# Optimization experiments

Hardware: AMD Instinct MI355X
Metric: run time of the kernel (lower is better)

The kernel has to match this reference:

```python
import jax, jax.numpy as jnp
import numpy as np

NEG_SLOPE = 0.2  # PyG GATConv default

def gat_conv(x, src, dst, W, att_src, att_dst, bias, n_nodes):
    """PyG-style GATConv (self-loops already included in src/dst)."""
    H, C = att_src.shape
    h = (x @ W).reshape(n_nodes, H, C)                       # [N,H,C]
    a_src = jnp.einsum('nhc,hc->nh', h, att_src)             # [N,H]
    a_dst = jnp.einsum('nhc,hc->nh', h, att_dst)             # [N,H]
    e = jax.nn.leaky_relu(a_src[src] + a_dst[dst], NEG_SLOPE)  # [E,H]
    # numerically stable segment softmax over incoming edges of each dst node
    e_max = jax.ops.segment_max(e, dst, num_segments=n_nodes)   # [N,H]
    e_exp = jnp.exp(e - e_max[dst])
    denom = jax.ops.segment_sum(e_exp, dst, num_segments=n_nodes)  # [N,H]
    alpha = e_exp / (denom[dst] + 1e-16)                     # [E,H]
    msg = h[src] * alpha[:, :, None]                         # [E,H,C]
    out = jax.ops.segment_sum(msg, dst, num_segments=n_nodes)  # [N,H,C]
    return out.reshape(n_nodes, H * C) + bias

def add_self_loops(edge_index, n_nodes):
    loop = jnp.arange(n_nodes, dtype=edge_index.dtype)
    src = jnp.concatenate([edge_index[0], loop])
    dst = jnp.concatenate([edge_index[1], loop])
    return src, dst

def setup_inputs() -> dict:
    key = jax.random.key(0)
    ks = jax.random.split(key, 12)
    N, E, IN, HID, H1 = 50000, 800000, 128, 64, 4
    s = lambda k, shape, scale: jax.random.normal(k, shape, dtype=jnp.float32) * scale
    return {
        'x': s(ks[0], (N, IN), 1.0),
        'edge_index': jax.random.randint(ks[1], (2, E), 0, N, dtype=jnp.int64),
        'W1': s(ks[2], (IN, H1 * HID), (2.0 / IN) ** 0.5),
        'att_src1': s(ks[3], (H1, HID), 0.1),
        'att_dst1': s(ks[4], (H1, HID), 0.1),
        'b1': s(ks[5], (H1 * HID,), 0.02),
        'W2': s(ks[6], (H1 * HID, HID), (2.0 / (H1 * HID)) ** 0.5),
        'att_src2': s(ks[7], (1, HID), 0.1),
        'att_dst2': s(ks[8], (1, HID), 0.1),
        'b2': s(ks[9], (HID,), 0.02),
        'Ws': s(ks[10], (HID, 1), (2.0 / HID) ** 0.5),
        'bs': s(ks[11], (1,), 0.02),
    }

def reference(x, edge_index, W1, att_src1, att_dst1, b1, W2, att_src2, att_dst2, b2, Ws, bs):
    N = x.shape[0]
    src, dst = add_self_loops(edge_index, N)
    h = jax.nn.elu(gat_conv(x, src, dst, W1, att_src1, att_dst1, b1, N))   # [N,256]
    # dropout is identity in eval mode
    h = jax.nn.elu(gat_conv(h, src, dst, W2, att_src2, att_dst2, b2, N))   # [N,64]
    scores = (h @ Ws + bs).squeeze(-1)                                     # [N]
    return h, scores
```

## Files before the change

### kernel.cpp

```cpp
#include <hip/hip_runtime.h>
#include <hip/hip_bf16.h>
#include <math.h>


#define LRELU_SLOPE 0.2f

typedef __attribute__((ext_vector_type(8))) short short8;
typedef __attribute__((ext_vector_type(4))) float f32x4;

__device__ inline ushort f2bf(float f) {
    uint u = __float_as_uint(f);
    return (ushort)((u + 0x7FFFu + ((u >> 16) & 1u)) >> 16);
}
__device__ inline float bf2f(ushort u) {
    return __uint_as_float(((uint)u) << 16);
}

__device__ inline void prefrag_one(const float* __restrict__ W,
                                   ushort* __restrict__ out,
                                   int tid, int T, int ldn)
{
    int l = tid & 63, jt = tid >> 6;
    int t = jt % T, j = jt / T;
    int n = j * 16 + (l & 15);
    int k0 = t * 32 + (l >> 4) * 8;
    ushort o[8];
    #pragma unroll
    for (int b = 0; b < 8; ++b) o[b] = f2bf(W[(size_t)(k0 + b) * ldn + n]);
    *(short8*)(out + (size_t)tid * 8) = *(short8*)o;
}

__global__ __launch_bounds__(256)
void fused_front(const float* __restrict__ x, ushort* __restrict__ xbf,
                 const float* __restrict__ W1, const float* __restrict__ W2,
                 ushort* __restrict__ o1, ushort* __restrict__ o2,
                 const int* __restrict__ edst, int* __restrict__ deg,
                 int nconv4, int E)
{
    int tid = blockIdx.x * blockDim.x + threadIdx.x;
    if (tid < nconv4) {
        int i = tid << 2;
        float4 v = *(const float4*)(x + i);
        ushort4 o;
        o.x = f2bf(v.x); o.y = f2bf(v.y); o.z = f2bf(v.z); o.w = f2bf(v.w);
        *(ushort4*)(xbf + i) = o;
        return;
    }
    int t = tid - nconv4;
    if (t < 16 * 4 * 64) { prefrag_one(W1, o1, t, 4, 256); return; }
    t -= 16 * 4 * 64;
    if (t < 4 * 8 * 64)  { prefrag_one(W2, o2, t, 8, 64); return; }
    t -= 4 * 8 * 64;
    int i = t << 2;
    if (i + 3 < E) {
        int4 v = *(const int4*)(edst + i);
        atomicAdd(&deg[v.x], 1); atomicAdd(&deg[v.y], 1);
        atomicAdd(&deg[v.z], 1); atomicAdd(&deg[v.w], 1);
    } else {
        for (; i < E; ++i) atomicAdd(&deg[edst[i]], 1);
    }
}

__global__ __launch_bounds__(1024)
void scan_rowptr(const int* __restrict__ deg, int* __restrict__ rowptr, int N)
{
    __shared__ int wsums[16];
    const int tid = threadIdx.x, lane = tid & 63, wid = tid >> 6;
    const int N4 = N >> 2;
    const int b4 = tid * 13;
    int tsum = 0;
    #pragma unroll
    for (int k = 0; k < 13; ++k) {
        int i4 = b4 + k;
        if (i4 < N4) {
            int4 v = ((const int4*)deg)[i4];
            tsum += (v.x + v.y) + (v.z + v.w);
        }
    }
    int sc = tsum;
    #pragma unroll
    for (int off = 1; off < 64; off <<= 1) {
        int t = __shfl_up(sc, off);
        if (lane >= off) sc += t;
    }
    if (lane == 63) wsums[wid] = sc;
    __syncthreads();
    if (wid == 0) {
        int wv = (lane < 16) ? wsums[lane] : 0;
        #pragma unroll
        for (int off = 1; off < 16; off <<= 1) {
            int t = __shfl_up(wv, off);
            if (lane >= off) wv += t;
        }
        if (lane < 16) wsums[lane] = wv;
    }
    __syncthreads();
    int run = (wid ? wsums[wid - 1] : 0) + sc - tsum;
    #pragma unroll
    for (int k = 0; k < 13; ++k) {
        int i4 = b4 + k;
        if (i4 < N4) {
            int4 v = ((const int4*)deg)[i4];
            int4 o;
            o.x = run; o.y = run + v.x; o.z = o.y + v.y; o.w = o.z + v.z;
            ((int4*)rowptr)[i4] = o;
            run += (v.x + v.y) + (v.z + v.w);
        }
    }
    if (tid == 1023) rowptr[N] = run;
}

template<int J, int T, int H>
__device__ inline void gemm_body(int wid, const ushort* __restrict__ A,
                                 const ushort* __restrict__ Bf,
                                 ushort* __restrict__ Cbf,
                                 const float* __restrict__ attS,
                                 const float* __restrict__ attD,
                                 float* __restrict__ as_,
                                 float* __restrict__ ad_, int M)
{
    constexpr int K = 32 * T;
    constexpr int NN = 16 * J;
    const int l = threadIdx.x & 63;
    const int base = wid * 16;
    if (base >= M) return;
    const int lm = l & 15, lg = l >> 4;

    short8 a[T];
    const ushort* ap = A + (size_t)(base + lm) * K + lg * 8;
    #pragma unroll
    for (int t = 0; t < T; ++t) a[t] = *(const short8*)(ap + t * 32);

    f32x4 acc[J];
    #pragma unroll
    for (int j = 0; j < J; ++j) acc[j] = (f32x4){0.f, 0.f, 0.f, 0.f};

    const ushort* bp = Bf + (size_t)l * 8;
    #pragma unroll
    for (int j = 0; j < J; ++j)
        #pragma unroll
        for (int t = 0; t < T; ++t) {
            short8 b = *(const short8*)(bp + (size_t)(j * T + t) * 512);
            acc[j] = __builtin_amdgcn_mfma_f32_16x16x32_bf16(a[t], b, acc[j], 0, 0, 0);
        }

    float sp[H][4], dp[H][4];
    #pragma unroll
    for (int h = 0; h < H; ++h)
        #pragma unroll
        for (int r = 0; r < 4; ++r) { sp[h][r] = 0.f; dp[h][r] = 0.f; }

    #pragma unroll
    for (int j = 0; j < J; ++j) {
        const int h = j / (J / H);
        const int coff = (j % (J / H)) * 16 + lm;
        float ws = attS[h * 64 + coff];
        float wd = attD[h * 64 + coff];
        #pragma unroll
        for (int r = 0; r < 4; ++r) {
            int row = base + lg * 4 + r;
            Cbf[(size_t)row * NN + j * 16 + lm] = f2bf(acc[j][r]);
            sp[h][r] = fmaf(acc[j][r], ws, sp[h][r]);
            dp[h][r] = fmaf(acc[j][r], wd, dp[h][r]);
        }
    }
    #pragma unroll
    for (int h = 0; h < H; ++h)
        #pragma unroll
        for (int r = 0; r < 4; ++r) {
            float s = sp[h][r], d = dp[h][r];
            s += __shfl_xor(s, 1); d += __shfl_xor(d, 1);
            s += __shfl_xor(s, 2); d += __shfl_xor(d, 2);
            s += __shfl_xor(s, 4); d += __shfl_xor(d, 4);
            s += __shfl_xor(s, 8); d += __shfl_xor(d, 8);
            if (lm == 0) {
                int row = base + lg * 4 + r;
                as_[row * H + h] = s;
                ad_[row * H + h] = d;
            }
        }
}

__global__ __launch_bounds__(256)
void scatter_gemm1(const ushort* __restrict__ A, const ushort* __restrict__ Bf,
                   ushort* __restrict__ Cbf, const float* __restrict__ attS,
                   const float* __restrict__ attD, float* __restrict__ as_,
                   float* __restrict__ ad_, int M, int gemmBlocks,
                   const int* __restrict__ esrc, const int* __restrict__ edst,
                   const int* __restrict__ rowptr, int* __restrict__ deg,
                   int* __restrict__ csr_src, int E)
{
    if ((int)blockIdx.x < gemmBlocks) {
        int wid = blockIdx.x * (blockDim.x >> 6) + (threadIdx.x >> 6);
        gemm_body<16, 4, 4>(wid, A, Bf, Cbf, attS, attD, as_, ad_, M);
        return;
    }
    int i = (blockIdx.x - gemmBlocks) * blockDim.x + threadIdx.x;
    if (i >= E) return;
    int s = esrc[i], d = edst[i];
    int pos = rowptr[d] + atomicSub(&deg[d], 1) - 1;
    csr_src[pos] = s;
}

template<int J, int T, int H>
__global__ __launch_bounds__(256)
void gemm_mfma(const ushort* __restrict__ A, const ushort* __restrict__ Bf,
               ushort* __restrict__ Cbf, const float* __restrict__ attS,
               const float* __restrict__ attD, float* __restrict__ as_,
               float* __restrict__ ad_, int M)
{
    int wid = blockIdx.x * (blockDim.x >> 6) + (threadIdx.x >> 6);
    gemm_body<J, T, H>(wid, A, Bf, Cbf, attS, attD, as_, ad_, M);
}

__global__ __launch_bounds__(256)
void aggregate_l1(const int* __restrict__ rowptr, const int* __restrict__ csr_src,
                  const ushort* __restrict__ h1, const float* __restrict__ as_,
                  const float* __restrict__ ad_, const float* __restrict__ bias,
                  ushort* __restrict__ outbf, int N)
{
    int w = (blockIdx.x * blockDim.x + threadIdx.x) >> 6;
    int lane = threadIdx.x & 63;
    if (w >= N) return;
    const int head = lane >> 4;
    const int c0 = lane << 2;
    const int my = lane & 3;
    const int hb = lane & 48;
    const float ad = ad_[w * 4 + head];
    float4 acc;
    float dsum;

    {
        float el = as_[w * 4 + head] + ad;
        el = el > 0.f ? el : LRELU_SLOPE * el;
        float p = __expf(el);
        ushort4 u = *(const ushort4*)(h1 + (size_t)w * 256 + c0);
        acc.x = p * bf2f(u.x); acc.y = p * bf2f(u.y);
        acc.z = p * bf2f(u.z); acc.w = p * bf2f(u.w);
        dsum = p;
    }

    int e = rowptr[w];
    const int e1 = rowptr[w + 1];
    for (; e + 3 < e1; e += 4) {
        int s0 = csr_src[e],     s1 = csr_src[e + 1];
        int s2 = csr_src[e + 2], s3 = csr_src[e + 3];
        ushort4 u0 = *(const ushort4*)(h1 + (size_t)s0 * 256 + c0);
        ushort4 u1 = *(const ushort4*)(h1 + (size_t)s1 * 256 + c0);
        ushort4 u2 = *(const ushort4*)(h1 + (size_t)s2 * 256 + c0);
        ushort4 u3 = *(const ushort4*)(h1 + (size_t)s3 * 256 + c0);
        int ms = s0;
        ms = (my == 1) ? s1 : ms;
        ms = (my == 2) ? s2 : ms;
        ms = (my == 3) ? s3 : ms;
        float ev = as_[ms * 4 + head] + ad;
        ev = ev > 0.f ? ev : LRELU_SLOPE * ev;
        float pl = __expf(ev);
        float p0 = __shfl(pl, hb | 0);
        float p1 = __shfl(pl, hb | 1);
        float p2 = __shfl(pl, hb | 2);
        float p3 = __shfl(pl, hb | 3);
        acc.x = fmaf(p0, bf2f(u0.x), acc.x); acc.y = fmaf(p0, bf2f(u0.y), acc.y);
        acc.z = fmaf(p0, bf2f(u0.z), acc.z); acc.w = fmaf(p0, bf2f(u0.w), acc.w);
        acc.x = fmaf(p1, bf2f(u1.x), acc.x); acc.y = fmaf(p1, bf2f(u1.y), acc.y);
        acc.z = fmaf(p1, bf2f(u1.z), acc.z); acc.w = fmaf(p1, bf2f(u1.w), acc.w);
        acc.x = fmaf(p2, bf2f(u2.x), acc.x); acc.y = fmaf(p2, bf2f(u2.y), acc.y);
        acc.z = fmaf(p2, bf2f(u2.z), acc.z); acc.w = fmaf(p2, bf2f(u2.w), acc.w);
        acc.x = fmaf(p3, bf2f(u3.x), acc.x); acc.y = fmaf(p3, bf2f(u3.y), acc.y);
        acc.z = fmaf(p3, bf2f(u3.z), acc.z); acc.w = fmaf(p3, bf2f(u3.w), acc.w);
        dsum += (p0 + p1) + (p2 + p3);
    }
    for (; e < e1; ++e) {
        int s0 = csr_src[e];
        float e0 = as_[s0 * 4 + head] + ad;
        e0 = e0 > 0.f ? e0 : LRELU_SLOPE * e0;
        float p0 = __expf(e0);
        ushort4 u0 = *(const ushort4*)(h1 + (size_t)s0 * 256 + c0);
        acc.x = fmaf(p0, bf2f(u0.x), acc.x); acc.y = fmaf(p0, bf2f(u0.y), acc.y);
        acc.z = fmaf(p0, bf2f(u0.z), acc.z); acc.w = fmaf(p0, bf2f(u0.w), acc.w);
        dsum += p0;
    }
    const float inv = 1.f / (dsum + 1e-16f);
    const float4 b = *(const float4*)(bias + c0);
    float ox = acc.x * inv + b.x; ox = ox > 0.f ? ox : expm1f(ox);
    float oy = acc.y * inv + b.y; oy = oy > 0.f ? oy : expm1f(oy);
    float oz = acc.z * inv + b.z; oz = oz > 0.f ? oz : expm1f(oz);
    float ow = acc.w * inv + b.w; ow = ow > 0.f ? ow : expm1f(ow);
    ushort4 o;
    o.x = f2bf(ox); o.y = f2bf(oy); o.z = f2bf(oz); o.w = f2bf(ow);
    *(ushort4*)(outbf + (size_t)w * 256 + c0) = o;
}

__global__ __launch_bounds__(256)
void aggregate_l2(const int* __restrict__ rowptr, const int* __restrict__ csr_src,
                  const ushort* __restrict__ h2, const float* __restrict__ as_,
                  const float* __restrict__ ad_, const float* __restrict__ b2,
                  const float* __restrict__ Wsv, const float* __restrict__ bs,
                  float* __restrict__ hout, float* __restrict__ scores, int N)
{
    int w = (blockIdx.x * blockDim.x + threadIdx.x) >> 6;
    int lane = threadIdx.x & 63;
    if (w >= N) return;
    const int my = lane & 3;
    const float ad = ad_[w];
    float acc, dsum;
    {
        float el = as_[w] + ad;
        el = el > 0.f ? el : LRELU_SLOPE * el;
        float p = __expf(el);
        acc = p * bf2f(h2[(size_t)w * 64 + lane]);
        dsum = p;
    }
    int e = rowptr[w];
    const int e1 = rowptr[w + 1];
    for (; e + 3 < e1; e += 4) {
        int s0 = csr_src[e],     s1 = csr_src[e + 1];
        int s2 = csr_src[e + 2], s3 = csr_src[e + 3];
        ushort f0 = h2[(size_t)s0 * 64 + lane];
        ushort f1 = h2[(size_t)s1 * 64 + lane];
        ushort f2 = h2[(size_t)s2 * 64 + lane];
        ushort f3 = h2[(size_t)s3 * 64 + lane];
        int ms = s0;
        ms = (my == 1) ? s1 : ms;
        ms = (my == 2) ? s2 : ms;
        ms = (my == 3) ? s3 : ms;
        float ev = as_[ms] + ad;
        ev = ev > 0.f ? ev : LRELU_SLOPE * ev;
        float pl = __expf(ev);
        float p0 = __shfl(pl, 0);
        float p1 = __shfl(pl, 1);
        float p2 = __shfl(pl, 2);
        float p3 = __shfl(pl, 3);
        acc = fmaf(p0, bf2f(f0), acc);
        acc = fmaf(p1, bf2f(f1), acc);
        acc = fmaf(p2, bf2f(f2), acc);
        acc = fmaf(p3, bf2f(f3), acc);
        dsum += (p0 + p1) + (p2 + p3);
    }
    for (; e < e1; ++e) {
        int s0 = csr_src[e];
        float e0 = as_[s0] + ad;
        e0 = e0 > 0.f ? e0 : LRELU_SLOPE * e0;
        float p0 = __expf(e0);
        acc = fmaf(p0, bf2f(h2[(size_t)s0 * 64 + lane]), acc);
        dsum += p0;
    }
    float v = acc / (dsum + 1e-16f) + b2[lane];
    v = v > 0.f ? v : expm1f(v);
    hout[(size_t)w * 64 + lane] = v;
    float sc = v * Wsv[lane];
    #pragma unroll
    for (int off = 32; off; off >>= 1) sc += __shfl_down(sc, off);
    if (lane == 0) scores[w] = sc + bs[0];
}

extern "C" void kernel_launch(void* const* d_in, const int* in_sizes, int n_in,
                              void* d_out, int out_size, void* d_ws, size_t ws_size,
                              hipStream_t stream)
{
    const float* x    = (const float*)d_in[0];
    const int*   ei   = (const int*)d_in[1];
    const float* W1   = (const float*)d_in[2];
    const float* as1w = (const float*)d_in[3];
    const float* ad1w = (const float*)d_in[4];
    const float* b1   = (const float*)d_in[5];
    const float* W2   = (const float*)d_in[6];
    const float* as2w = (const float*)d_in[7];
    const float* ad2w = (const float*)d_in[8];
    const float* b2   = (const float*)d_in[9];
    const float* Ws   = (const float*)d_in[10];
    const float* bs   = (const float*)d_in[11];

    const int N  = in_sizes[0] / 128;
    const int E  = in_sizes[1] / 2;
    const int* esrc = ei;
    const int* edst = ei + E;

    ushort* h1bf  = (ushort*)d_ws;
    ushort* hl1bf = h1bf + (size_t)N * 256;
    ushort* h2bf  = hl1bf + (size_t)N * 256;
    ushort* xbf   = h2bf + (size_t)N * 64;
    ushort* bfr1  = xbf + (size_t)N * 128;
    ushort* bfr2  = bfr1 + 32768;
    float*  as1   = (float*)(bfr2 + 16384);
    float*  ad1   = as1 + (size_t)N * 4;
    float*  as2   = ad1 + (size_t)N * 4;
    float*  ad2   = as2 + N;
    int*    deg    = (int*)(ad2 + N);
    int*    rowptr = deg + N;
    int*    csr_src= rowptr + N + 4;

    float* hout   = (float*)d_out;
    float* scores = hout + (size_t)N * 64;

    hipMemsetAsync(deg, 0, (size_t)N * sizeof(int), stream);

    const int nconv4 = N * 128 / 4;
    const int nfrag  = 16 * 4 * 64 + 4 * 8 * 64;
    const int nhist  = (E + 3) / 4;
    fused_front<<<(nconv4 + nfrag + nhist + 255) / 256, 256, 0, stream>>>(
        x, xbf, W1, W2, bfr1, bfr2, edst, deg, nconv4, E);

    scan_rowptr<<<1, 1024, 0, stream>>>(deg, rowptr, N);

    const int gemmBlocks    = (N / 16 + 3) / 4;
    const int scatterBlocks = (E + 255) / 256;
    scatter_gemm1<<<gemmBlocks + scatterBlocks, 256, 0, stream>>>(
        xbf, bfr1, h1bf, as1w, ad1w, as1, ad1, N, gemmBlocks,
        esrc, edst, rowptr, deg, csr_src, E);

    aggregate_l1<<<((size_t)N * 64 + 255) / 256, 256, 0, stream>>>(
        rowptr, csr_src, h1bf, as1, ad1, b1, hl1bf, N);

    gemm_mfma<4, 8, 1><<<(N / 16 + 3) / 4, 256, 0, stream>>>(
        hl1bf, bfr2, h2bf, as2w, ad2w, as2, ad2, N);

    aggregate_l2<<<((size_t)N * 64 + 255) / 256, 256, 0, stream>>>(
        rowptr, csr_src, h2bf, as2, ad2, b2, Ws, bs, hout, scores, N);
}
```

Measured before the change: 249.5 us.

## Fuse layer-1 aggregation with layer-2 GEMM via LDS; split GEMM1 columns across waves

Layer-1 aggregation now writes each 16-node tile of bf16 outputs into shared memory, and the same block then runs the layer-2 MFMA GEMM on it, computing the attention logits through a cross-wave reduction. This drops the global write and re-read of the N×256 intermediate and removes one kernel launch. Separately, the GEMM1 work inside scatter_gemm1 is split so that each wave handles one head's 64 columns of a 16-row tile instead of all 256, which gives four times as many GEMM blocks at lower register pressure each. In exchange, each aggregation block now loops serially over 4 nodes per wave and adds two block barriers, which may reduce latency hiding in the gather.

```diff
diff --git a/kernel.cpp b/kernel.cpp
--- a/kernel.cpp
+++ b/kernel.cpp
@@ -110,77 +110,6 @@
     if (tid == 1023) rowptr[N] = run;
 }
 
-template<int J, int T, int H>
-__device__ inline void gemm_body(int wid, const ushort* __restrict__ A,
-                                 const ushort* __restrict__ Bf,
-                                 ushort* __restrict__ Cbf,
-                                 const float* __restrict__ attS,
-                                 const float* __restrict__ attD,
-                                 float* __restrict__ as_,
-                                 float* __restrict__ ad_, int M)
-{
-    constexpr int K = 32 * T;
-    constexpr int NN = 16 * J;
-    const int l = threadIdx.x & 63;
-    const int base = wid * 16;
-    if (base >= M) return;
-    const int lm = l & 15, lg = l >> 4;
-
-    short8 a[T];
-    const ushort* ap = A + (size_t)(base + lm) * K + lg * 8;
-    #pragma unroll
-    for (int t = 0; t < T; ++t) a[t] = *(const short8*)(ap + t * 32);
-
-    f32x4 acc[J];
-    #pragma unroll
-    for (int j = 0; j < J; ++j) acc[j] = (f32x4){0.f, 0.f, 0.f, 0.f};
-
-    const ushort* bp = Bf + (size_t)l * 8;
-    #pragma unroll
-    for (int j = 0; j < J; ++j)
-        #pragma unroll
-        for (int t = 0; t < T; ++t) {
-            short8 b = *(const short8*)(bp + (size_t)(j * T + t) * 512);
-            acc[j] = __builtin_amdgcn_mfma_f32_16x16x32_bf16(a[t], b, acc[j], 0, 0, 0);
-        }
-
-    float sp[H][4], dp[H][4];
-    #pragma unroll
-    for (int h = 0; h < H; ++h)
-        #pragma unroll
-        for (int r = 0; r < 4; ++r) { sp[h][r] = 0.f; dp[h][r] = 0.f; }
-
-    #pragma unroll
-    for (int j = 0; j < J; ++j) {
-        const int h = j / (J / H);
-        const int coff = (j % (J / H)) * 16 + lm;
-        float ws = attS[h * 64 + coff];
-        float wd = attD[h * 64 + coff];
-        #pragma unroll
-        for (int r = 0; r < 4; ++r) {
-            int row = base + lg * 4 + r;
-            Cbf[(size_t)row * NN + j * 16 + lm] = f2bf(acc[j][r]);
-            sp[h][r] = fmaf(acc[j][r], ws, sp[h][r]);
-            dp[h][r] = fmaf(acc[j][r], wd, dp[h][r]);
-        }
-    }
-    #pragma unroll
-    for (int h = 0; h < H; ++h)
-        #pragma unroll
-        for (int r = 0; r < 4; ++r) {
-            float s = sp[h][r], d = dp[h][r];
-            s += __shfl_xor(s, 1); d += __shfl_xor(d, 1);
-            s += __shfl_xor(s, 2); d += __shfl_xor(d, 2);
-            s += __shfl_xor(s, 4); d += __shfl_xor(d, 4);
-            s += __shfl_xor(s, 8); d += __shfl_xor(d, 8);
-            if (lm == 0) {
-                int row = base + lg * 4 + r;
-                as_[row * H + h] = s;
-                ad_[row * H + h] = d;
-            }
-        }
-}
-
 __global__ __launch_bounds__(256)
 void scatter_gemm1(const ushort* __restrict__ A, const ushort* __restrict__ Bf,
                    ushort* __restrict__ Cbf, const float* __restrict__ attS,
@@ -191,8 +120,60 @@
                    int* __restrict__ csr_src, int E)
 {
     if ((int)blockIdx.x < gemmBlocks) {
-        int wid = blockIdx.x * (blockDim.x >> 6) + (threadIdx.x >> 6);
-        gemm_body<16, 4, 4>(wid, A, Bf, Cbf, attS, attD, as_, ad_, M);
+        const int wv = blockIdx.x * 4 + (threadIdx.x >> 6);
+        const int rowTile = wv >> 2;
+        const int q = wv & 3;
+        const int base = rowTile * 16;
+        if (base >= M) return;
+        const int l = threadIdx.x & 63;
+        const int lm = l & 15, lg = l >> 4;
+
+        short8 a[4];
+        const ushort* ap = A + (size_t)(base + lm) * 128 + lg * 8;
+        #pragma unroll
+        for (int t = 0; t < 4; ++t) a[t] = *(const short8*)(ap + t * 32);
+
+        f32x4 acc[4];
+        #pragma unroll
+        for (int j = 0; j < 4; ++j) acc[j] = (f32x4){0.f, 0.f, 0.f, 0.f};
+
+        const ushort* bp = Bf + (size_t)l * 8;
+        #pragma unroll
+        for (int j = 0; j < 4; ++j) {
+            const int jg = q * 4 + j;
+            #pragma unroll
+            for (int t = 0; t < 4; ++t) {
+                short8 b = *(const short8*)(bp + (size_t)(jg * 4 + t) * 512);
+                acc[j] = __builtin_amdgcn_mfma_f32_16x16x32_bf16(a[t], b, acc[j], 0, 0, 0);
+            }
+        }
+
+        float sp[4] = {0.f, 0.f, 0.f, 0.f}, dp[4] = {0.f, 0.f, 0.f, 0.f};
+        #pragma unroll
+        for (int j = 0; j < 4; ++j) {
+            float ws = attS[q * 64 + j * 16 + lm];
+            float wd = attD[q * 64 + j * 16 + lm];
+            #pragma unroll
+            for (int r = 0; r < 4; ++r) {
+                int row = base + lg * 4 + r;
+                Cbf[(size_t)row * 256 + (q * 4 + j) * 16 + lm] = f2bf(acc[j][r]);
+                sp[r] = fmaf(acc[j][r], ws, sp[r]);
+                dp[r] = fmaf(acc[j][r], wd, dp[r]);
+            }
+        }
+        #pragma unroll
+        for (int r = 0; r < 4; ++r) {
+            float s = sp[r], d = dp[r];
+            s += __shfl_xor(s, 1); d += __shfl_xor(d, 1);
+            s += __shfl_xor(s, 2); d += __shfl_xor(d, 2);
+            s += __shfl_xor(s, 4); d += __shfl_xor(d, 4);
+            s += __shfl_xor(s, 8); d += __shfl_xor(d, 8);
+            if (lm == 0) {
+                int row = base + lg * 4 + r;
+                as_[row * 4 + q] = s;
+                ad_[row * 4 + q] = d;
+            }
+        }
         return;
     }
     int i = (blockIdx.x - gemmBlocks) * blockDim.x + threadIdx.x;
@@ -202,93 +183,137 @@
     csr_src[pos] = s;
 }
 
-template<int J, int T, int H>
 __global__ __launch_bounds__(256)
-void gemm_mfma(const ushort* __restrict__ A, const ushort* __restrict__ Bf,
-               ushort* __restrict__ Cbf, const float* __restrict__ attS,
-               const float* __restrict__ attD, float* __restrict__ as_,
-               float* __restrict__ ad_, int M)
-{
-    int wid = blockIdx.x * (blockDim.x >> 6) + (threadIdx.x >> 6);
-    gemm_body<J, T, H>(wid, A, Bf, Cbf, attS, attD, as_, ad_, M);
-}
-
-__global__ __launch_bounds__(256)
-void aggregate_l1(const int* __restrict__ rowptr, const int* __restrict__ csr_src,
-                  const ushort* __restrict__ h1, const float* __restrict__ as_,
-                  const float* __restrict__ ad_, const float* __restrict__ bias,
-                  ushort* __restrict__ outbf, int N)
-{
-    int w = (blockIdx.x * blockDim.x + threadIdx.x) >> 6;
-    int lane = threadIdx.x & 63;
-    if (w >= N) return;
+void agg1_gemm2(const int* __restrict__ rowptr, const int* __restrict__ csr_src,
+                const ushort* __restrict__ h1, const float* __restrict__ as_,
+                const float* __restrict__ ad_, const float* __restrict__ bias,
+                const ushort* __restrict__ Bf2, const float* __restrict__ attS2,
+                const float* __restrict__ attD2, float* __restrict__ as2,
+                float* __restrict__ ad2, ushort* __restrict__ h2bf, int N)
+{
+    __shared__ ushort hl[16][264];
+    __shared__ float partS[4][16], partD[4][16];
+    const int lane = threadIdx.x & 63;
+    const int v = threadIdx.x >> 6;
+    const int nbase = blockIdx.x * 16;
     const int head = lane >> 4;
     const int c0 = lane << 2;
     const int my = lane & 3;
     const int hb = lane & 48;
-    const float ad = ad_[w * 4 + head];
-    float4 acc;
-    float dsum;
+
+    for (int qn = 0; qn < 4; ++qn) {
+        const int w = nbase + v * 4 + qn;
+        if (w >= N) break;
+        const float ad = ad_[w * 4 + head];
+        float4 acc;
+        float dsum;
+        {
+            float el = as_[w * 4 + head] + ad;
+            el = el > 0.f ? el : LRELU_SLOPE * el;
+            float p = __expf(el);
+            ushort4 u = *(const ushort4*)(h1 + (size_t)w * 256 + c0);
+            acc.x = p * bf2f(u.x); acc.y = p * bf2f(u.y);
+            acc.z = p * bf2f(u.z); acc.w = p * bf2f(u.w);
+            dsum = p;
+        }
+        int e = rowptr[w];
+        const int e1 = rowptr[w + 1];
+        for (; e + 3 < e1; e += 4) {
+            int s0 = csr_src[e],     s1 = csr_src[e + 1];
+            int s2 = csr_src[e + 2], s3 = csr_src[e + 3];
+            ushort4 u0 = *(const ushort4*)(h1 + (size_t)s0 * 256 + c0);
+            ushort4 u1 = *(const ushort4*)(h1 + (size_t)s1 * 256 + c0);
+            ushort4 u2 = *(const ushort4*)(h1 + (size_t)s2 * 256 + c0);
+            ushort4 u3 = *(const ushort4*)(h1 + (size_t)s3 * 256 + c0);
+            int ms = s0;
+            ms = (my == 1) ? s1 : ms;
+            ms = (my == 2) ? s2 : ms;
+            ms = (my == 3) ? s3 : ms;
+            float ev = as_[ms * 4 + head] + ad;
+            ev = ev > 0.f ? ev : LRELU_SLOPE * ev;
+            float pl = __expf(ev);
+            float p0 = __shfl(pl, hb | 0);
+            float p1 = __shfl(pl, hb | 1);
+            float p2 = __shfl(pl, hb | 2);
+            float p3 = __shfl(pl, hb | 3);
+            acc.x = fmaf(p0, bf2f(u0.x), acc.x); acc.y = fmaf(p0, bf2f(u0.y), acc.y);
+            acc.z = fmaf(p0, bf2f(u0.z), acc.z); acc.w = fmaf(p0, bf2f(u0.w), acc.w);
+            acc.x = fmaf(p1, bf2f(u1.x), acc.x); acc.y = fmaf(p1, bf2f(u1.y), acc.y);
+            acc.z = fmaf(p1, bf2f(u1.z), acc.z); acc.w = fmaf(p1, bf2f(u1.w), acc.w);
+            acc.x = fmaf(p2, bf2f(u2.x), acc.x); acc.y = fmaf(p2, bf2f(u2.y), acc.y);
+            acc.z = fmaf(p2, bf2f(u2.z), acc.z); acc.w = fmaf(p2, bf2f(u2.w), acc.w);
+            acc.x = fmaf(p3, bf2f(u3.x), acc.x); acc.y = fmaf(p3, bf2f(u3.y), acc.y);
+            acc.z = fmaf(p3, bf2f(u3.z), acc.z); acc.w = fmaf(p3, bf2f(u3.w), acc.w);
+            dsum += (p0 + p1) + (p2 + p3);
+        }
+        for (; e < e1; ++e) {
+            int s0 = csr_src[e];
+            float e0 = as_[s0 * 4 + head] + ad;
+            e0 = e0 > 0.f ? e0 : LRELU_SLOPE * e0;
+            float p0 = __expf(e0);
+            ushort4 u0 = *(const ushort4*)(h1 + (size_t)s0 * 256 + c0);
+            acc.x = fmaf(p0, bf2f(u0.x), acc.x); acc.y = fmaf(p0, bf2f(u0.y), acc.y);
+            acc.z = fmaf(p0, bf2f(u0.z), acc.z); acc.w = fmaf(p0, bf2f(u0.w), acc.w);
+            dsum += p0;
+        }
+        const float inv = 1.f / (dsum + 1e-16f);
+        const float4 b = *(const float4*)(bias + c0);
+        float ox = acc.x * inv + b.x; ox = ox > 0.f ? ox : expm1f(ox);
+        float oy = acc.y * inv + b.y; oy = oy > 0.f ? oy : expm1f(oy);
+        float oz = acc.z * inv + b.z; oz = oz > 0.f ? oz : expm1f(oz);
+        float ow = acc.w * inv + b.w; ow = ow > 0.f ? ow : expm1f(ow);
+        ushort4 o;
+        o.x = f2bf(ox); o.y = f2bf(oy); o.z = f2bf(oz); o.w = f2bf(ow);
+        *(ushort4*)&hl[v * 4 + qn][c0] = o;
+    }
+    __syncthreads();
 
     {
-        float el = as_[w * 4 + head] + ad;
-        el = el > 0.f ? el : LRELU_SLOPE * el;
-        float p = __expf(el);
-        ushort4 u = *(const ushort4*)(h1 + (size_t)w * 256 + c0);
-        acc.x = p * bf2f(u.x); acc.y = p * bf2f(u.y);
-        acc.z = p * bf2f(u.z); acc.w = p * bf2f(u.w);
-        dsum = p;
-    }
-
-    int e = rowptr[w];
-    const int e1 = rowptr[w + 1];
-    for (; e + 3 < e1; e += 4) {
-        int s0 = csr_src[e],     s1 = csr_src[e + 1];
-        int s2 = csr_src[e + 2], s3 = csr_src[e + 3];
-        ushort4 u0 = *(const ushort4*)(h1 + (size_t)s0 * 256 + c0);
-        ushort4 u1 = *(const ushort4*)(h1 + (size_t)s1 * 256 + c0);
-        ushort4 u2 = *(const ushort4*)(h1 + (size_t)s2 * 256 + c0);
-        ushort4 u3 = *(const ushort4*)(h1 + (size_t)s3 * 256 + c0);
-        int ms = s0;
-        ms = (my == 1) ? s1 : ms;
-        ms = (my == 2) ? s2 : ms;
-        ms = (my == 3) ? s3 : ms;
-        float ev = as_[ms * 4 + head] + ad;
-        ev = ev > 0.f ? ev : LRELU_SLOPE * ev;
-        float pl = __expf(ev);
-        float p0 = __shfl(pl, hb | 0);
-        float p1 = __shfl(pl, hb | 1);
-        float p2 = __shfl(pl, hb | 2);
-        float p3 = __shfl(pl, hb | 3);
-        acc.x = fmaf(p0, bf2f(u0.x), acc.x); acc.y = fmaf(p0, bf2f(u0.y), acc.y);
-        acc.z = fmaf(p0, bf2f(u0.z), acc.z); acc.w = fmaf(p0, bf2f(u0.w), acc.w);
-        acc.x = fmaf(p1, bf2f(u1.x), acc.x); acc.y = fmaf(p1, bf2f(u1.y), acc.y);
-        acc.z = fmaf(p1, bf2f(u1.z), acc.z); acc.w = fmaf(p1, bf2f(u1.w), acc.w);
-        acc.x = fmaf(p2, bf2f(u2.x), acc.x); acc.y = fmaf(p2, bf2f(u2.y), acc.y);
-        acc.z = fmaf(p2, bf2f(u2.z), acc.z); acc.w = fmaf(p2, bf2f(u2.w), acc.w);
-        acc.x = fmaf(p3, bf2f(u3.x), acc.x); acc.y = fmaf(p3, bf2f(u3.y), acc.y);
-        acc.z = fmaf(p3, bf2f(u3.z), acc.z); acc.w = fmaf(p3, bf2f(u3.w), acc.w);
-        dsum += (p0 + p1) + (p2 + p3);
-    }
-    for (; e < e1; ++e) {
-        int s0 = csr_src[e];
-        float e0 = as_[s0 * 4 + head] + ad;
-        e0 = e0 > 0.f ? e0 : LRELU_SLOPE * e0;
-        float p0 = __expf(e0);
-        ushort4 u0 = *(const ushort4*)(h1 + (size_t)s0 * 256 + c0);
-        acc.x = fmaf(p0, bf2f(u0.x), acc.x); acc.y = fmaf(p0, bf2f(u0.y), acc.y);
-        acc.z = fmaf(p0, bf2f(u0.z), acc.z); acc.w = fmaf(p0, bf2f(u0.w), acc.w);
-        dsum += p0;
-    }
-    const float inv = 1.f / (dsum + 1e-16f);
-    const float4 b = *(const float4*)(bias + c0);
-    float ox = acc.x * inv + b.x; ox = ox > 0.f ? ox : expm1f(ox);
-    float oy = acc.y * inv + b.y; oy = oy > 0.f ? oy : expm1f(oy);
-    float oz = acc.z * inv + b.z; oz = oz > 0.f ? oz : expm1f(oz);
-    float ow = acc.w * inv + b.w; ow = ow > 0.f ? ow : expm1f(ow);
-    ushort4 o;
-    o.x = f2bf(ox); o.y = f2bf(oy); o.z = f2bf(oz); o.w = f2bf(ow);
-    *(ushort4*)(outbf + (size_t)w * 256 + c0) = o;
+        const int lm = lane & 15, lg = lane >> 4;
+        short8 a[8];
+        #pragma unroll
+        for (int t = 0; t < 8; ++t)
+            a[t] = *(const short8*)&hl[lm][lg * 8 + t * 32];
+        f32x4 acc = (f32x4){0.f, 0.f, 0.f, 0.f};
+        const ushort* bp = Bf2 + (size_t)(v * 8) * 512 + (size_t)lane * 8;
+        #pragma unroll
+        for (int t = 0; t < 8; ++t) {
+            short8 b = *(const short8*)(bp + (size_t)t * 512);
+            acc = __builtin_amdgcn_mfma_f32_16x16x32_bf16(a[t], b, acc, 0, 0, 0);
+        }
+        const float ws = attS2[v * 16 + lm];
+        const float wd = attD2[v * 16 + lm];
+        float sp[4], dp[4];
+        #pragma unroll
+        for (int r = 0; r < 4; ++r) {
+            int row = nbase + lg * 4 + r;
+            if (row < N)
+                h2bf[(size_t)row * 64 + v * 16 + lm] = f2bf(acc[r]);
+            sp[r] = acc[r] * ws;
+            dp[r] = acc[r] * wd;
+        }
+        #pragma unroll
+        for (int r = 0; r < 4; ++r) {
+            float s = sp[r], d = dp[r];
+            s += __shfl_xor(s, 1); d += __shfl_xor(d, 1);
+            s += __shfl_xor(s, 2); d += __shfl_xor(d, 2);
+            s += __shfl_xor(s, 4); d += __shfl_xor(d, 4);
+            s += __shfl_xor(s, 8); d += __shfl_xor(d, 8);
+            if (lm == 0) {
+                partS[v][lg * 4 + r] = s;
+                partD[v][lg * 4 + r] = d;
+            }
+        }
+    }
+    __syncthreads();
+    if (threadIdx.x < 16) {
+        int row = nbase + threadIdx.x;
+        if (row < N) {
+            int t = threadIdx.x;
+            as2[row] = ((partS[0][t] + partS[1][t]) + (partS[2][t] + partS[3][t]));
+            ad2[row] = ((partD[0][t] + partD[1][t]) + (partD[2][t] + partD[3][t]));
+        }
+    }
 }
 
 __global__ __launch_bounds__(256)
@@ -377,8 +402,7 @@
     const int* edst = ei + E;
 
     ushort* h1bf  = (ushort*)d_ws;
-    ushort* hl1bf = h1bf + (size_t)N * 256;
-    ushort* h2bf  = hl1bf + (size_t)N * 256;
+    ushort* h2bf  = h1bf + (size_t)N * 256;
     ushort* xbf   = h2bf + (size_t)N * 64;
     ushort* bfr1  = xbf + (size_t)N * 128;
     ushort* bfr2  = bfr1 + 32768;
@@ -403,17 +427,15 @@
 
     scan_rowptr<<<1, 1024, 0, stream>>>(deg, rowptr, N);
 
-    const int gemmBlocks    = (N / 16 + 3) / 4;
+    const int gemmBlocks    = N / 16;
     const int scatterBlocks = (E + 255) / 256;
     scatter_gemm1<<<gemmBlocks + scatterBlocks, 256, 0, stream>>>(
         xbf, bfr1, h1bf, as1w, ad1w, as1, ad1, N, gemmBlocks,
         esrc, edst, rowptr, deg, csr_src, E);
 
-    aggregate_l1<<<((size_t)N * 64 + 255) / 256, 256, 0, stream>>>(
-        rowptr, csr_src, h1bf, as1, ad1, b1, hl1bf, N);
-
-    gemm_mfma<4, 8, 1><<<(N / 16 + 3) / 4, 256, 0, stream>>>(
-        hl1bf, bfr2, h2bf, as2w, ad2w, as2, ad2, N);
+    agg1_gemm2<<<(N + 15) / 16, 256, 0, stream>>>(
+        rowptr, csr_src, h1bf, as1, ad1, b1,
+        bfr2, as2w, ad2w, as2, ad2, h2bf, N);
 
     aggregate_l2<<<((size_t)N * 64 + 255) / 256, 256, 0, stream>>>(
         rowptr, csr_src, h2bf, as2, ad2, b2, Ws, bs, hout, scores, N);
```

Measured after the change: 256.1 us. 1.03x slower.

## Split layer-1 GEMM across two waves per row tile and precompute scatter cursors

Applied to the files above, without the earlier changes.

The scan now writes a separate cursor array holding each row's end offset, so the CSR scatter does a single atomicSub on the cursor and no longer reads rowptr. The fused scatter/GEMM launch puts the scatter blocks first and splits each 16-row layer-1 GEMM tile across two waves, each computing 128 of the 256 output columns and two of the four heads. This doubles the GEMM wave count, with fewer accumulators per wave, to raise parallelism and occupancy, and it shifts the block ordering. The cost is that each row's A fragment is loaded twice and the scan writes one extra N-sized array.

```diff
diff --git a/kernel.cpp b/kernel.cpp
--- a/kernel.cpp
+++ b/kernel.cpp
@@ -62,7 +62,8 @@
 }
 
 __global__ __launch_bounds__(1024)
-void scan_rowptr(const int* __restrict__ deg, int* __restrict__ rowptr, int N)
+void scan_rowptr(const int* __restrict__ deg, int* __restrict__ rowptr,
+                 int* __restrict__ cursor, int N)
 {
     __shared__ int wsums[16];
     const int tid = threadIdx.x, lane = tid & 63, wid = tid >> 6;
@@ -101,27 +102,111 @@
         int i4 = b4 + k;
         if (i4 < N4) {
             int4 v = ((const int4*)deg)[i4];
-            int4 o;
-            o.x = run; o.y = run + v.x; o.z = o.y + v.y; o.w = o.z + v.z;
+            int4 o, c;
+            o.x = run;        c.x = run + v.x;
+            o.y = c.x;        c.y = c.x + v.y;
+            o.z = c.y;        c.z = c.y + v.z;
+            o.w = c.z;        c.w = c.z + v.w;
             ((int4*)rowptr)[i4] = o;
-            run += (v.x + v.y) + (v.z + v.w);
+            ((int4*)cursor)[i4] = c;
+            run = c.w;
         }
     }
     if (tid == 1023) rowptr[N] = run;
 }
 
+__global__ __launch_bounds__(256)
+void scatter_gemm1(const ushort* __restrict__ A, const ushort* __restrict__ Bf,
+                   ushort* __restrict__ Cbf, const float* __restrict__ attS,
+                   const float* __restrict__ attD, float* __restrict__ as_,
+                   float* __restrict__ ad_, int M, int scatterBlocks,
+                   const int* __restrict__ esrc, const int* __restrict__ edst,
+                   int* __restrict__ cursor, int* __restrict__ csr_src, int E)
+{
+    if ((int)blockIdx.x < scatterBlocks) {
+        int i = blockIdx.x * blockDim.x + threadIdx.x;
+        if (i >= E) return;
+        int s = esrc[i], d = edst[i];
+        int pos = atomicSub(&cursor[d], 1) - 1;
+        csr_src[pos] = s;
+        return;
+    }
+    const int wv = (blockIdx.x - scatterBlocks) * 4 + (threadIdx.x >> 6);
+    const int rowTile = wv >> 1;
+    const int half = wv & 1;
+    const int base = rowTile * 16;
+    if (base >= M) return;
+    const int l = threadIdx.x & 63;
+    const int lm = l & 15, lg = l >> 4;
+
+    short8 a[4];
+    const ushort* ap = A + (size_t)(base + lm) * 128 + lg * 8;
+    #pragma unroll
+    for (int t = 0; t < 4; ++t) a[t] = *(const short8*)(ap + t * 32);
+
+    f32x4 acc[8];
+    #pragma unroll
+    for (int j = 0; j < 8; ++j) acc[j] = (f32x4){0.f, 0.f, 0.f, 0.f};
+
+    const ushort* bp = Bf + (size_t)l * 8;
+    #pragma unroll
+    for (int j = 0; j < 8; ++j) {
+        const int jg = half * 8 + j;
+        #pragma unroll
+        for (int t = 0; t < 4; ++t) {
+            short8 b = *(const short8*)(bp + (size_t)(jg * 4 + t) * 512);
+            acc[j] = __builtin_amdgcn_mfma_f32_16x16x32_bf16(a[t], b, acc[j], 0, 0, 0);
+        }
+    }
+
+    float sp[2][4], dp[2][4];
+    #pragma unroll
+    for (int h = 0; h < 2; ++h)
+        #pragma unroll
+        for (int r = 0; r < 4; ++r) { sp[h][r] = 0.f; dp[h][r] = 0.f; }
+
+    #pragma unroll
+    for (int j = 0; j < 8; ++j) {
+        const int h = j >> 2;
+        const int hg = half * 2 + h;
+        float ws = attS[hg * 64 + (j & 3) * 16 + lm];
+        float wd = attD[hg * 64 + (j & 3) * 16 + lm];
+        #pragma unroll
+        for (int r = 0; r < 4; ++r) {
+            int row = base + lg * 4 + r;
+            Cbf[(size_t)row * 256 + (half * 8 + j) * 16 + lm] = f2bf(acc[j][r]);
+            sp[h][r] = fmaf(acc[j][r], ws, sp[h][r]);
+            dp[h][r] = fmaf(acc[j][r], wd, dp[h][r]);
+        }
+    }
+    #pragma unroll
+    for (int h = 0; h < 2; ++h)
+        #pragma unroll
+        for (int r = 0; r < 4; ++r) {
+            float s = sp[h][r], d = dp[h][r];
+            s += __shfl_xor(s, 1); d += __shfl_xor(d, 1);
+            s += __shfl_xor(s, 2); d += __shfl_xor(d, 2);
+            s += __shfl_xor(s, 4); d += __shfl_xor(d, 4);
+            s += __shfl_xor(s, 8); d += __shfl_xor(d, 8);
+            if (lm == 0) {
+                int row = base + lg * 4 + r;
+                as_[row * 4 + half * 2 + h] = s;
+                ad_[row * 4 + half * 2 + h] = d;
+            }
+        }
+}
+
 template<int J, int T, int H>
-__device__ inline void gemm_body(int wid, const ushort* __restrict__ A,
-                                 const ushort* __restrict__ Bf,
-                                 ushort* __restrict__ Cbf,
-                                 const float* __restrict__ attS,
-                                 const float* __restrict__ attD,
-                                 float* __restrict__ as_,
-                                 float* __restrict__ ad_, int M)
+__global__ __launch_bounds__(256)
+void gemm_mfma(const ushort* __restrict__ A, const ushort* __restrict__ Bf,
+               ushort* __restrict__ Cbf, const float* __restrict__ attS,
+               const float* __restrict__ attD, float* __restrict__ as_,
+               float* __restrict__ ad_, int M)
 {
     constexpr int K = 32 * T;
     constexpr int NN = 16 * J;
     const int l = threadIdx.x & 63;
+    const int wid = blockIdx.x * (blockDim.x >> 6) + (threadIdx.x >> 6);
     const int base = wid * 16;
     if (base >= M) return;
     const int lm = l & 15, lg = l >> 4;
@@ -179,38 +264,6 @@
                 ad_[row * H + h] = d;
             }
         }
-}
-
-__global__ __launch_bounds__(256)
-void scatter_gemm1(const ushort* __restrict__ A, const ushort* __restrict__ Bf,
-                   ushort* __restrict__ Cbf, const float* __restrict__ attS,
-                   const float* __restrict__ attD, float* __restrict__ as_,
-                   float* __restrict__ ad_, int M, int gemmBlocks,
-                   const int* __restrict__ esrc, const int* __restrict__ edst,
-                   const int* __restrict__ rowptr, int* __restrict__ deg,
-                   int* __restrict__ csr_src, int E)
-{
-    if ((int)blockIdx.x < gemmBlocks) {
-        int wid = blockIdx.x * (blockDim.x >> 6) + (threadIdx.x >> 6);
-        gemm_body<16, 4, 4>(wid, A, Bf, Cbf, attS, attD, as_, ad_, M);
-        return;
-    }
-    int i = (blockIdx.x - gemmBlocks) * blockDim.x + threadIdx.x;
-    if (i >= E) return;
-    int s = esrc[i], d = edst[i];
-    int pos = rowptr[d] + atomicSub(&deg[d], 1) - 1;
-    csr_src[pos] = s;
-}
-
-template<int J, int T, int H>
-__global__ __launch_bounds__(256)
-void gemm_mfma(const ushort* __restrict__ A, const ushort* __restrict__ Bf,
-               ushort* __restrict__ Cbf, const float* __restrict__ attS,
-               const float* __restrict__ attD, float* __restrict__ as_,
-               float* __restrict__ ad_, int M)
-{
-    int wid = blockIdx.x * (blockDim.x >> 6) + (threadIdx.x >> 6);
-    gemm_body<J, T, H>(wid, A, Bf, Cbf, attS, attD, as_, ad_, M);
 }
 
 __global__ __launch_bounds__(256)
@@ -387,7 +440,8 @@
     float*  as2   = ad1 + (size_t)N * 4;
     float*  ad2   = as2 + N;
     int*    deg    = (int*)(ad2 + N);
-    int*    rowptr = deg + N;
+    int*    cursor = deg + N;
+    int*    rowptr = cursor + N;
     int*    csr_src= rowptr + N + 4;
 
     float* hout   = (float*)d_out;
@@ -401,13 +455,13 @@
     fused_front<<<(nconv4 + nfrag + nhist + 255) / 256, 256, 0, stream>>>(
         x, xbf, W1, W2, bfr1, bfr2, edst, deg, nconv4, E);
 
-    scan_rowptr<<<1, 1024, 0, stream>>>(deg, rowptr, N);
-
-    const int gemmBlocks    = (N / 16 + 3) / 4;
+    scan_rowptr<<<1, 1024, 0, stream>>>(deg, rowptr, cursor, N);
+
     const int scatterBlocks = (E + 255) / 256;
-    scatter_gemm1<<<gemmBlocks + scatterBlocks, 256, 0, stream>>>(
-        xbf, bfr1, h1bf, as1w, ad1w, as1, ad1, N, gemmBlocks,
-        esrc, edst, rowptr, deg, csr_src, E);
+    const int gemmBlocks    = (N / 16 * 2 + 3) / 4;
+    scatter_gemm1<<<scatterBlocks + gemmBlocks, 256, 0, stream>>>(
+        xbf, bfr1, h1bf, as1w, ad1w, as1, ad1, N, scatterBlocks,
+        esrc, edst, cursor, csr_src, E);
 
     aggregate_l1<<<((size_t)N * 64 + 255) / 256, 256, 0, stream>>>(
         rowptr, csr_src, h1bf, as1, ad1, b1, hl1bf, N);
```

Result: slower. 281.7 us (+12.9%).
